# Kernel tuning notes

Measured on AMD Instinct MI355X. Metric: run time of the kernel, lower is better.

The kernel has to match this reference:

```python
import jax, jax.numpy as jnp
import numpy as np

# Globals from the original script
H_MAX = 10.0
TIMESTEP = 0.01
NUM_SAMPLES = int(H_MAX / TIMESTEP) + 1  # 1001
TRAIN_TD_MAX = 100.0
EMBED_DIM = 32
NUM_NODES = 50000
BATCH = 512


def hawkes_intensity(z_u, z_v, et_uv, td, W, b, psi, alpha, w_t):
    """Faithful to Decoder.hawkes_intensity (symmetric=False branch).
    z_u, z_v: (..., D) broadcastable; et_uv, td broadcastable to output shape.
    The per-event-type masked-linear loop is equivalent to computing both
    1-output linears and selecting by event type.
    """
    D = z_u.shape[-1]
    Wu, Wv = W[:, :D], W[:, D:]  # split Linear(2D -> 1) weights (2, D) each
    et = (et_uv > 0).astype(jnp.int32)
    td_norm = td / TRAIN_TD_MAX
    # g for both event types, broadcast-added instead of materializing cat(z_u, z_v)
    g01 = jnp.matmul(z_u, Wu.T) + jnp.matmul(z_v, Wv.T) + b  # (..., 2)
    g = jnp.where(et == 1, g01[..., 1], g01[..., 0])
    psi_e = psi[et]
    alpha_e = alpha[et]
    w_t_e = w_t[et]
    g = g + alpha_e * jnp.exp(-w_t_e * td_norm)
    g_psi = g / (psi_e + 1e-7)
    # log(1 + exp(-g_psi)) + g_psi, computed stably
    return psi_e * (jnp.logaddexp(0.0, -g_psi) + g_psi)


def setup_inputs() -> dict:
    key = jax.random.key(0)
    ks = jax.random.split(key, 12)
    N, B, D = NUM_NODES, BATCH, EMBED_DIM
    all_embeddings = jax.random.normal(ks[0], (N, D), dtype=jnp.float32)
    assoc = jnp.arange(N, dtype=jnp.int32)  # identity mapping node id -> memory slot
    src = jax.random.randint(ks[1], (B,), 0, N)
    pos_dst = jax.random.randint(ks[2], (B,), 0, N)
    neg_dst = jax.random.randint(ks[3], (B,), 0, N)
    et = jax.random.randint(ks[4], (B,), 0, 2)
    last_update = jax.random.uniform(ks[5], (N,), dtype=jnp.float32) * 50.0
    cur_time = jax.random.uniform(ks[6], (B,), dtype=jnp.float32) * 50.0 + 50.0
    # Linear(2D -> 1) weights for the two event types, stacked: (2, 2D), bias (2,)
    W = jax.random.normal(ks[7], (2, 2 * D), dtype=jnp.float32) / np.sqrt(2 * D)
    b = jax.random.normal(ks[8], (2,), dtype=jnp.float32) * 0.01
    psi = 0.5 * jnp.ones((2,), dtype=jnp.float32)
    alpha = jax.random.uniform(ks[9], (2,), dtype=jnp.float32)
    w_t = jax.random.uniform(ks[10], (2,), dtype=jnp.float32)
    return {"all_embeddings": all_embeddings, "assoc": assoc, "src": src,
            "pos_dst": pos_dst, "neg_dst": neg_dst, "last_update": last_update,
            "cur_time": cur_time, "et": et, "W": W, "b": b, "psi": psi,
            "alpha": alpha, "w_t": w_t}


def reference(all_embeddings, assoc, src, pos_dst, neg_dst, last_update,
              cur_time, et, W, b, psi, alpha, w_t):
    z_src = all_embeddings[assoc[src]]        # (B, D)
    z_dst = all_embeddings[assoc[pos_dst]]    # (B, D)
    td_src = cur_time - last_update[assoc[src]]   # (B,)
    td_dst = cur_time - last_update[assoc[pos_dst]]

    # lambda over all candidate nodes; broadcasting replaces the huge .repeat()
    lambda_src = hawkes_intensity(z_src[:, None, :], all_embeddings[None, :, :],
                                  et[:, None], td_src[:, None],
                                  W, b, psi, alpha, w_t)      # (B, N)
    lambda_dst = hawkes_intensity(all_embeddings[None, :, :], z_dst[:, None, :],
                                  et[:, None], td_dst[:, None],
                                  W, b, psi, alpha, w_t)      # (B, N)

    # return-time prediction via unit-time sampling integral
    all_td = jnp.linspace(0.0, H_MAX, NUM_SAMPLES).astype(jnp.float32)  # (S,)
    # symmetric=True averages two identical calls -> compute once
    intensity = hawkes_intensity(z_src[None, :, :], z_dst[None, :, :],
                                 et[None, :], all_td[:, None],
                                 W, b, psi, alpha, w_t)       # (S, B)
    integral = jnp.cumsum(TIMESTEP * intensity, axis=0)
    density = intensity * jnp.exp(-integral)
    t_sample = all_td[:, None] * density                      # (S, B)
    return_time_pred = (TIMESTEP * 0.5 * (t_sample[:-1] + t_sample[1:])).sum(axis=0)  # (B,)
    return lambda_src, lambda_dst, return_time_pred
```

## Files before the change

### kernel.cpp

```cpp
#include <hip/hip_runtime.h>

#define N_NODES 50000
#define BATCH   512
#define DIM     32
#define LOG2E 1.4426950408889634f
#define LN2   0.6931471805599453f
#define A1C 0.996829f
#define A2C (-0.441666f)
#define A3C 0.139730f

typedef float vfloat4 __attribute__((ext_vector_type(4)));

__global__ void prep_kernel(const float* __restrict__ emb,
                            const int*   __restrict__ assoc,
                            const int*   __restrict__ src,
                            const int*   __restrict__ pdst,
                            const float* __restrict__ last_update,
                            const float* __restrict__ cur_time,
                            const int*   __restrict__ et,
                            const float* __restrict__ W,
                            const float* __restrict__ bias,
                            const float* __restrict__ psi,
                            const float* __restrict__ alpha,
                            const float* __restrict__ w_t,
                            float* __restrict__ nv0, float* __restrict__ nv1,
                            float* __restrict__ nu0, float* __restrict__ nu1,
                            float* __restrict__ pb) {
    if (blockIdx.x < 196) {
        int n = blockIdx.x * 256 + threadIdx.x;
        if (n >= N_NODES) return;
        const float4* e4 = (const float4*)(emb + (size_t)n * DIM);
        float u0 = 0.f, u1 = 0.f, v0 = 0.f, v1 = 0.f;
#pragma unroll
        for (int q = 0; q < 8; ++q) {
            float4 v = e4[q];
            int d = q * 4;
            u0 += v.x * W[d]      + v.y * W[d + 1]      + v.z * W[d + 2]      + v.w * W[d + 3];
            v0 += v.x * W[32 + d] + v.y * W[32 + d + 1] + v.z * W[32 + d + 2] + v.w * W[32 + d + 3];
            u1 += v.x * W[64 + d] + v.y * W[64 + d + 1] + v.z * W[64 + d + 2] + v.w * W[64 + d + 3];
            v1 += v.x * W[96 + d] + v.y * W[96 + d + 1] + v.z * W[96 + d + 2] + v.w * W[96 + d + 3];
        }
        nu0[n] = u0; nu1[n] = u1; nv0[n] = v0; nv1[n] = v1;
    } else {
        int b = (blockIdx.x - 196) * 256 + threadIdx.x;
        if (b >= BATCH) return;
        int e  = (et[b] > 0) ? 1 : 0;
        int is = assoc[src[b]];
        int id = assoc[pdst[b]];
        const float4* Wu = (const float4*)(W + e * 64);
        const float4* Wv = (const float4*)(W + e * 64 + 32);
        const float4* zs = (const float4*)(emb + (size_t)is * DIM);
        const float4* zd = (const float4*)(emb + (size_t)id * DIM);
        float su = 0.f, dv = 0.f;
#pragma unroll
        for (int q = 0; q < 8; ++q) {
            float4 a = zs[q], wa = Wu[q];
            float4 c = zd[q], wc = Wv[q];
            su += a.x * wa.x + a.y * wa.y + a.z * wa.z + a.w * wa.w;
            dv += c.x * wc.x + c.y * wc.y + c.z * wc.z + c.w * wc.w;
        }
        float ct  = cur_time[b];
        float tds = (ct - last_update[is]) * 0.01f;
        float tdd = (ct - last_update[id]) * 0.01f;
        float al = alpha[e], wt = w_t[e], bb = bias[e], ps = psi[e];
        float ip  = 1.0f / (ps + 1e-7f);
        float ipl = ip * LOG2E;
        float bs = su + bb + al * __expf(-wt * tds);
        float bd = dv + bb + al * __expf(-wt * tdd);
        float* p = pb + (size_t)b * 16;
        p[0]  = bs * ipl;
        p[1]  = bd * ipl;
        p[2]  = ipl;
        p[3]  = ps * LN2;
        p[4]  = ps * A1C;
        p[5]  = ps * A2C;
        p[6]  = ps * A3C;
        p[7]  = (float)e;
        p[8]  = su + dv + bb;
        p[9]  = al;
        p[10] = wt;
        p[11] = ps;
        p[12] = ip;
        p[13] = 0.f; p[14] = 0.f; p[15] = 0.f;
    }
}

__global__ void __launch_bounds__(256) main_kernel(
        const float* __restrict__ nv0, const float* __restrict__ nv1,
        const float* __restrict__ nu0, const float* __restrict__ nu1,
        const float* __restrict__ pb,
        float* __restrict__ out) {
    __shared__ float wsum[4];
    __shared__ float bred[4];
    int b = blockIdx.y;
    const float* p = pb + (size_t)b * 16;

    if (blockIdx.x < 25) {
        int n8 = blockIdx.x * 256 + threadIdx.x;
        if (n8 >= N_NODES / 8) return;
        const float4* p4 = (const float4*)p;
        float4 pa = p4[0];
        float4 pc = p4[1];
        float bsl = pa.x, bdl = pa.y, ipl = pa.z, C1 = pa.w;
        float A1p = pc.x, A2p = pc.y, A3p = pc.z;
        int e = (pc.w != 0.f);
        const float4* nvp = (const float4*)(e ? nv1 : nv0) + (size_t)n8 * 2;
        const float4* nup = (const float4*)(e ? nu1 : nu0) + (size_t)n8 * 2;
        float4 nva = nvp[0], nvb = nvp[1];
        float4 nua = nup[0], nub = nup[1];
        auto f = [&](float nvx, float base) {
            float xl = fmaf(nvx, ipl, base);
            float t  = __builtin_amdgcn_exp2f(-fabsf(xl));
            float pp = fmaf(t, A3p, A2p);
            pp = fmaf(t, pp, A1p);
            float m = fmaxf(xl, 0.f);
            return fmaf(pp, t, m * C1);
        };
        float4 osa, osb, oda, odb;
        osa.x = f(nva.x, bsl); osa.y = f(nva.y, bsl); osa.z = f(nva.z, bsl); osa.w = f(nva.w, bsl);
        osb.x = f(nvb.x, bsl); osb.y = f(nvb.y, bsl); osb.z = f(nvb.z, bsl); osb.w = f(nvb.w, bsl);
        oda.x = f(nua.x, bdl); oda.y = f(nua.y, bdl); oda.z = f(nua.z, bdl); oda.w = f(nua.w, bdl);
        odb.x = f(nub.x, bdl); odb.y = f(nub.y, bdl); odb.z = f(nub.z, bdl); odb.w = f(nub.w, bdl);
        float4* os_out = (float4*)(out + (size_t)b * N_NODES) + (size_t)n8 * 2;
        float4* od_out = (float4*)(out + (size_t)(BATCH + b) * N_NODES) + (size_t)n8 * 2;
        os_out[0] = osa; os_out[1] = osb;
        od_out[0] = oda; od_out[1] = odb;
    } else {
        float bint = p[8], al = p[9], wt = p[10], ps = p[11], ip = p[12];
        int tid = threadIdx.x;
        int lane = tid & 63, wv = tid >> 6;
        float inten[4], c[4];
        float cum = 0.f;
#pragma unroll
        for (int i = 0; i < 4; ++i) {
            int t = tid * 4 + i;
            float x = (bint + al * __expf(-wt * (float)t * 1e-4f)) * ip;
            float v = ps * (__logf(1.0f + __expf(-fabsf(x))) + fmaxf(x, 0.0f));
            if (t > 1000) v = 0.f;
            inten[i] = v;
            cum += 0.01f * v;
            c[i] = cum;
        }
        float tot = cum;
#pragma unroll
        for (int off = 1; off < 64; off <<= 1) {
            float u = __shfl_up(tot, off, 64);
            if (lane >= off) tot += u;
        }
        if (lane == 63) wsum[wv] = tot;
        __syncthreads();
        float wpre = 0.f;
#pragma unroll
        for (int w = 0; w < 4; ++w) if (w < wv) wpre += wsum[w];
        float excl = wpre + tot - cum;
        float acc = 0.f;
#pragma unroll
        for (int i = 0; i < 4; ++i) {
            int t = tid * 4 + i;
            float integral = excl + c[i];
            float dens = inten[i] * __expf(-integral);
            float w = (t == 0 || t == 1000) ? 0.005f : (t < 1000 ? 0.01f : 0.f);
            acc += w * (float)t * 0.01f * dens;
        }
#pragma unroll
        for (int off = 32; off > 0; off >>= 1) acc += __shfl_down(acc, off, 64);
        if (lane == 0) bred[wv] = acc;
        __syncthreads();
        if (tid == 0)
            out[(size_t)2 * BATCH * N_NODES + b] = bred[0] + bred[1] + bred[2] + bred[3];
    }
}

extern "C" void kernel_launch(void* const* d_in, const int* in_sizes, int n_in,
                              void* d_out, int out_size, void* d_ws, size_t ws_size,
                              hipStream_t stream) {
    const float* emb         = (const float*)d_in[0];
    const int*   assoc       = (const int*)  d_in[1];
    const int*   src         = (const int*)  d_in[2];
    const int*   pdst        = (const int*)  d_in[3];
    const float* last_update = (const float*)d_in[5];
    const float* cur_time    = (const float*)d_in[6];
    const int*   et          = (const int*)  d_in[7];
    const float* W           = (const float*)d_in[8];
    const float* bias        = (const float*)d_in[9];
    const float* psi         = (const float*)d_in[10];
    const float* alpha       = (const float*)d_in[11];
    const float* w_t         = (const float*)d_in[12];
    float* out = (float*)d_out;

    float* ws  = (float*)d_ws;
    float* nv0 = ws;
    float* nv1 = ws + 50000;
    float* nu0 = ws + 100000;
    float* nu1 = ws + 150000;
    float* pb  = ws + 200000;

    prep_kernel<<<198, 256, 0, stream>>>(emb, assoc, src, pdst, last_update, cur_time,
                                         et, W, bias, psi, alpha, w_t,
                                         nv0, nv1, nu0, nu1, pb);
    dim3 grid(26, BATCH);
    main_kernel<<<grid, 256, 0, stream>>>(nv0, nv1, nu0, nu1, pb, out);
}
```

Measured before the change: 231.2 us.

## Process eight batch rows per block to reuse node projections in registers

Each main-kernel block now loads all four per-node projection vectors once and loops over eight batch rows, picking the right pair per row by event type. Previously each block reloaded the selected projections for a single batch row. Node indexing also changes to one float4 per thread per half-block, so neighbouring threads read and write neighbouring float4s. The return-time scan block now loops serially over eight rows with repeated barriers. The grid shrinks by a factor of eight, which trades fewer redundant loads for less parallelism and more registers per thread.

```diff
diff --git a/kernel.cpp b/kernel.cpp
--- a/kernel.cpp
+++ b/kernel.cpp
@@ -92,82 +92,101 @@
         float* __restrict__ out) {
     __shared__ float wsum[4];
     __shared__ float bred[4];
-    int b = blockIdx.y;
-    const float* p = pb + (size_t)b * 16;
+    int tid = threadIdx.x;
 
     if (blockIdx.x < 25) {
-        int n8 = blockIdx.x * 256 + threadIdx.x;
-        if (n8 >= N_NODES / 8) return;
-        const float4* p4 = (const float4*)p;
-        float4 pa = p4[0];
-        float4 pc = p4[1];
-        float bsl = pa.x, bdl = pa.y, ipl = pa.z, C1 = pa.w;
-        float A1p = pc.x, A2p = pc.y, A3p = pc.z;
-        int e = (pc.w != 0.f);
-        const float4* nvp = (const float4*)(e ? nv1 : nv0) + (size_t)n8 * 2;
-        const float4* nup = (const float4*)(e ? nu1 : nu0) + (size_t)n8 * 2;
-        float4 nva = nvp[0], nvb = nvp[1];
-        float4 nua = nup[0], nub = nup[1];
-        auto f = [&](float nvx, float base) {
-            float xl = fmaf(nvx, ipl, base);
-            float t  = __builtin_amdgcn_exp2f(-fabsf(xl));
-            float pp = fmaf(t, A3p, A2p);
-            pp = fmaf(t, pp, A1p);
-            float m = fmaxf(xl, 0.f);
-            return fmaf(pp, t, m * C1);
-        };
-        float4 osa, osb, oda, odb;
-        osa.x = f(nva.x, bsl); osa.y = f(nva.y, bsl); osa.z = f(nva.z, bsl); osa.w = f(nva.w, bsl);
-        osb.x = f(nvb.x, bsl); osb.y = f(nvb.y, bsl); osb.z = f(nvb.z, bsl); osb.w = f(nvb.w, bsl);
-        oda.x = f(nua.x, bdl); oda.y = f(nua.y, bdl); oda.z = f(nua.z, bdl); oda.w = f(nua.w, bdl);
-        odb.x = f(nub.x, bdl); odb.y = f(nub.y, bdl); odb.z = f(nub.z, bdl); odb.w = f(nub.w, bdl);
-        float4* os_out = (float4*)(out + (size_t)b * N_NODES) + (size_t)n8 * 2;
-        float4* od_out = (float4*)(out + (size_t)(BATCH + b) * N_NODES) + (size_t)n8 * 2;
-        os_out[0] = osa; os_out[1] = osb;
-        od_out[0] = oda; od_out[1] = odb;
+        int i0 = blockIdx.x * 512 + tid;
+        int i1 = i0 + 256;
+        bool ok0 = i0 < (N_NODES / 4);
+        bool ok1 = i1 < (N_NODES / 4);
+        int j0 = ok0 ? i0 : 0;
+        int j1 = ok1 ? i1 : 0;
+        const float4* nv0_4 = (const float4*)nv0;
+        const float4* nv1_4 = (const float4*)nv1;
+        const float4* nu0_4 = (const float4*)nu0;
+        const float4* nu1_4 = (const float4*)nu1;
+        float4 nv0a = nv0_4[j0], nv0b = nv0_4[j1];
+        float4 nv1a = nv1_4[j0], nv1b = nv1_4[j1];
+        float4 nu0a = nu0_4[j0], nu0b = nu0_4[j1];
+        float4 nu1a = nu1_4[j0], nu1b = nu1_4[j1];
+
+#pragma unroll
+        for (int bi = 0; bi < 8; ++bi) {
+            int b = blockIdx.y * 8 + bi;
+            const float4* p4 = (const float4*)(pb + (size_t)b * 16);
+            float4 pa = p4[0];
+            float4 pc = p4[1];
+            float bsl = pa.x, bdl = pa.y, ipl = pa.z, C1 = pa.w;
+            float A1p = pc.x, A2p = pc.y, A3p = pc.z;
+            bool e = (pc.w != 0.f);
+            float4 nva = e ? nv1a : nv0a;
+            float4 nvb = e ? nv1b : nv0b;
+            float4 nua = e ? nu1a : nu0a;
+            float4 nub = e ? nu1b : nu0b;
+            auto f = [&](float nvx, float base) {
+                float xl = fmaf(nvx, ipl, base);
+                float t  = __builtin_amdgcn_exp2f(-fabsf(xl));
+                float pp = fmaf(t, A3p, A2p);
+                pp = fmaf(t, pp, A1p);
+                float m = fmaxf(xl, 0.f);
+                return fmaf(pp, t, m * C1);
+            };
+            float4 osa, osb, oda, odb;
+            osa.x = f(nva.x, bsl); osa.y = f(nva.y, bsl); osa.z = f(nva.z, bsl); osa.w = f(nva.w, bsl);
+            osb.x = f(nvb.x, bsl); osb.y = f(nvb.y, bsl); osb.z = f(nvb.z, bsl); osb.w = f(nvb.w, bsl);
+            oda.x = f(nua.x, bdl); oda.y = f(nua.y, bdl); oda.z = f(nua.z, bdl); oda.w = f(nua.w, bdl);
+            odb.x = f(nub.x, bdl); odb.y = f(nub.y, bdl); odb.z = f(nub.z, bdl); odb.w = f(nub.w, bdl);
+            float4* orow = (float4*)out + (size_t)b * (N_NODES / 4);
+            float4* drow = (float4*)out + (size_t)(BATCH + b) * (N_NODES / 4);
+            if (ok0) { orow[i0] = osa; drow[i0] = oda; }
+            if (ok1) { orow[i1] = osb; drow[i1] = odb; }
+        }
     } else {
-        float bint = p[8], al = p[9], wt = p[10], ps = p[11], ip = p[12];
-        int tid = threadIdx.x;
-        int lane = tid & 63, wv = tid >> 6;
-        float inten[4], c[4];
-        float cum = 0.f;
-#pragma unroll
-        for (int i = 0; i < 4; ++i) {
-            int t = tid * 4 + i;
-            float x = (bint + al * __expf(-wt * (float)t * 1e-4f)) * ip;
-            float v = ps * (__logf(1.0f + __expf(-fabsf(x))) + fmaxf(x, 0.0f));
-            if (t > 1000) v = 0.f;
-            inten[i] = v;
-            cum += 0.01f * v;
-            c[i] = cum;
-        }
-        float tot = cum;
-#pragma unroll
-        for (int off = 1; off < 64; off <<= 1) {
-            float u = __shfl_up(tot, off, 64);
-            if (lane >= off) tot += u;
-        }
-        if (lane == 63) wsum[wv] = tot;
-        __syncthreads();
-        float wpre = 0.f;
-#pragma unroll
-        for (int w = 0; w < 4; ++w) if (w < wv) wpre += wsum[w];
-        float excl = wpre + tot - cum;
-        float acc = 0.f;
-#pragma unroll
-        for (int i = 0; i < 4; ++i) {
-            int t = tid * 4 + i;
-            float integral = excl + c[i];
-            float dens = inten[i] * __expf(-integral);
-            float w = (t == 0 || t == 1000) ? 0.005f : (t < 1000 ? 0.01f : 0.f);
-            acc += w * (float)t * 0.01f * dens;
-        }
-#pragma unroll
-        for (int off = 32; off > 0; off >>= 1) acc += __shfl_down(acc, off, 64);
-        if (lane == 0) bred[wv] = acc;
-        __syncthreads();
-        if (tid == 0)
-            out[(size_t)2 * BATCH * N_NODES + b] = bred[0] + bred[1] + bred[2] + bred[3];
+        for (int bi = 0; bi < 8; ++bi) {
+            int b = blockIdx.y * 8 + bi;
+            const float* p = pb + (size_t)b * 16;
+            float bint = p[8], al = p[9], wt = p[10], ps = p[11], ip = p[12];
+            int lane = tid & 63, wv = tid >> 6;
+            float inten[4], c[4];
+            float cum = 0.f;
+#pragma unroll
+            for (int i = 0; i < 4; ++i) {
+                int t = tid * 4 + i;
+                float x = (bint + al * __expf(-wt * (float)t * 1e-4f)) * ip;
+                float v = ps * (__logf(1.0f + __expf(-fabsf(x))) + fmaxf(x, 0.0f));
+                if (t > 1000) v = 0.f;
+                inten[i] = v;
+                cum += 0.01f * v;
+                c[i] = cum;
+            }
+            float tot = cum;
+#pragma unroll
+            for (int off = 1; off < 64; off <<= 1) {
+                float u = __shfl_up(tot, off, 64);
+                if (lane >= off) tot += u;
+            }
+            if (lane == 63) wsum[wv] = tot;
+            __syncthreads();
+            float wpre = 0.f;
+#pragma unroll
+            for (int w = 0; w < 4; ++w) if (w < wv) wpre += wsum[w];
+            float excl = wpre + tot - cum;
+            float acc = 0.f;
+#pragma unroll
+            for (int i = 0; i < 4; ++i) {
+                int t = tid * 4 + i;
+                float integral = excl + c[i];
+                float dens = inten[i] * __expf(-integral);
+                float w = (t == 0 || t == 1000) ? 0.005f : (t < 1000 ? 0.01f : 0.f);
+                acc += w * (float)t * 0.01f * dens;
+            }
+#pragma unroll
+            for (int off = 32; off > 0; off >>= 1) acc += __shfl_down(acc, off, 64);
+            if (lane == 0) bred[wv] = acc;
+            __syncthreads();
+            if (tid == 0)
+                out[(size_t)2 * BATCH * N_NODES + b] = bred[0] + bred[1] + bred[2] + bred[3];
+        }
     }
 }
 
@@ -198,6 +217,6 @@
     prep_kernel<<<198, 256, 0, stream>>>(emb, assoc, src, pdst, last_update, cur_time,
                                          et, W, bias, psi, alpha, w_t,
                                          nv0, nv1, nu0, nu1, pb);
-    dim3 grid(26, BATCH);
+    dim3 grid(26, 64);
     main_kernel<<<grid, 256, 0, stream>>>(nv0, nv1, nu0, nu1, pb, out);
 }
```

New measurement: 233.5 us. No clear change (+1.0%).
